# Kernel tuning notes

Measured on AMD Instinct MI355X. Metric: run time of the kernel, lower is better.

Reference implementation:

```python
import jax, jax.numpy as jnp
import numpy as np

B, L, D, H, F, NL = 112, 128, 768, 12, 3072, 3
E = D // H  # head dim = 64
BN_EPS = 1e-5


def _bn(x, gamma, beta):
    # torch BatchNorm1d applied on x.permute(0,2,1): per-channel (d_model) stats over batch+seq
    mean = jnp.mean(x, axis=(0, 1), keepdims=True)
    var = jnp.var(x, axis=(0, 1), keepdims=True)
    return (x - mean) * jax.lax.rsqrt(var + BN_EPS) * gamma + beta


def setup_inputs() -> dict:
    key = jax.random.key(0)
    ks = jax.random.split(key, 10)
    s = 0.02
    inp = {
        "x": jax.random.normal(ks[0], (B, L, D), jnp.float32),
        "attn_bias": jax.random.normal(ks[1], (B, L, L, H), jnp.float32) * 0.1,
        "Wq": jax.random.normal(ks[2], (NL, D, D), jnp.float32) * s,
        "bq": jnp.zeros((NL, D), jnp.float32),
        "Wk": jax.random.normal(ks[3], (NL, D, D), jnp.float32) * s,
        "bk": jnp.zeros((NL, D), jnp.float32),
        "Wv": jax.random.normal(ks[4], (NL, D, D), jnp.float32) * s,
        "bv": jnp.zeros((NL, D), jnp.float32),
        "Wo": jax.random.normal(ks[5], (NL, D, D), jnp.float32) * s,
        "bo": jnp.zeros((NL, D), jnp.float32),
        "W1": jax.random.normal(ks[6], (NL, F, D), jnp.float32) * s,  # conv1 k=1 == Linear
        "b1": jnp.zeros((NL, F), jnp.float32),
        "W2": jax.random.normal(ks[7], (NL, D, F), jnp.float32) * s,  # conv2 k=1 == Linear
        "b2": jnp.zeros((NL, D), jnp.float32),
        "g1": jnp.ones((NL, D), jnp.float32),
        "be1": jnp.zeros((NL, D), jnp.float32),
        "g2": jnp.ones((NL, D), jnp.float32),
        "be2": jnp.zeros((NL, D), jnp.float32),
        "gf": jnp.ones((D,), jnp.float32),
        "bef": jnp.zeros((D,), jnp.float32),
    }
    return inp


def reference(x, attn_bias, Wq, bq, Wk, bk, Wv, bv, Wo, bo,
              W1, b1, W2, b2, g1, be1, g2, be2, gf, bef):
    scale = 1.0 / float(np.sqrt(E))
    bias_bhls = jnp.transpose(attn_bias, (0, 3, 1, 2))  # [B,H,L,S]
    for l in range(NL):
        q = (x @ Wq[l].T + bq[l]).reshape(B, L, H, E)
        k = (x @ Wk[l].T + bk[l]).reshape(B, L, H, E)
        v = (x @ Wv[l].T + bv[l]).reshape(B, L, H, E)
        scores = jnp.einsum('blhe,bshe->bhls', q, k)  # O(L^2) score tensor
        A = jax.nn.softmax(scores * scale + bias_bhls, axis=-1)
        V = jnp.einsum('bhls,bshd->blhd', A, v).reshape(B, L, D)
        new_x = V @ Wo[l].T + bo[l]
        x = _bn(x + new_x, g1[l], be1[l])
        y = jax.nn.gelu(x @ W1[l].T + b1[l], approximate=False)
        y = y @ W2[l].T + b2[l]
        x = _bn(x + y, g2[l], be2[l])
    return _bn(x, gf, bef)  # Encoder final BatchNorm1d(d_model)
```

## Files before the change

### kernel.cpp

```cpp
#include <hip/hip_runtime.h>

#define NB 112
#define SEQ 128
#define DM 768
#define NH 12
#define HD 64
#define FF 3072
#define NLAYER 3
#define MTOK (NB*SEQ)
#define QKVN (3*DM)
#define HEADTOT (NB*NH)
#define QSZ ((size_t)HEADTOT*SEQ*HD)

typedef unsigned short u16;
typedef __attribute__((ext_vector_type(8))) short short8;
typedef __attribute__((ext_vector_type(4))) float f32x4;
typedef __attribute__((ext_vector_type(4))) unsigned short us4;

__device__ __forceinline__ u16 f2bf(float f){
  unsigned u = __builtin_bit_cast(unsigned, f);
  u += 0x7FFFu + ((u >> 16) & 1u);
  return (u16)(u >> 16);
}
__device__ __forceinline__ float bf2f(u16 b){
  unsigned u = ((unsigned)b) << 16;
  return __builtin_bit_cast(float, u);
}
__device__ __forceinline__ unsigned cvt_pk_bf16(float lo, float hi){
  unsigned r;
  asm("v_cvt_pk_bf16_f32 %0, %1, %2" : "=v"(r) : "v"(lo), "v"(hi));
  return r;
}
__device__ __forceinline__ float gelu_t(float x){
  const float t = -1.5957691216057308f * x * __builtin_fmaf(0.044715f, x*x, 1.0f);
  return __fdividef(x, 1.0f + __expf(t));
}

__device__ __forceinline__ void gl_lds16(const void* g, void* l){
  __builtin_amdgcn_global_load_lds((const __attribute__((address_space(1))) unsigned*)g,
                                   (__attribute__((address_space(3))) unsigned*)l, 16, 0, 0);
}

template<int EPI>
__global__ __launch_bounds__(512, 1)
void gemm_bt(const u16* __restrict__ A, const u16* __restrict__ W,
             const float* __restrict__ bias, u16* __restrict__ obf,
             float* __restrict__ of32, const u16* __restrict__ res,
             float* __restrict__ p1, float* __restrict__ p2,
             int M, int N, int K, int Nt, int TPB)
{
  __shared__ __align__(16) char smem[163840];
  const int tid = threadIdx.x;
  const int w = tid >> 6, lane = tid & 63;
  const int wm = w >> 2, wn = w & 3;
  const int fr = lane & 15, fg = lane >> 4;
  const int fko = fg * 8;
  const int grid = gridDim.x;
  const int q8 = grid >> 3, r8 = grid & 7;
  const int xcd = blockIdx.x & 7, pos = blockIdx.x >> 3;
  const int start = xcd < r8 ? xcd * (q8 + 1) : r8 * (q8 + 1) + (xcd - r8) * q8;
  const int swz = start + pos;
  const int nt = K >> 6;
  const int tot = TPB * nt;
  const int l3 = lane >> 3;
  const int k16s = ((lane & 7) ^ l3) * 8;
  int rowAK[2][2], rowBK[2][2];
  #pragma unroll
  for (int mh = 0; mh < 2; mh++)
    #pragma unroll
    for (int j = 0; j < 2; j++)
      rowAK[mh][j] = (mh*64 + j*128 + w*8 + l3) * K;
  #pragma unroll
  for (int h = 0; h < 2; h++)
    #pragma unroll
    for (int j = 0; j < 2; j++)
      rowBK[h][j] = (h*128 + (w + j*8)*8 + l3) * K;

  auto stA = [&](int s, int soff) {
    #pragma unroll
    for (int mh = 0; mh < 2; mh++) {
      char* d = smem + s*32768 + (mh*64 + w*8)*128;
      gl_lds16(A + (size_t)soff + rowAK[mh][0] + k16s, d);
      gl_lds16(A + (size_t)soff + rowAK[mh][1] + k16s, d + 16384);
    }
  };
  auto stB = [&](int s, int soff) {
    #pragma unroll
    for (int h = 0; h < 2; h++) {
      char* d = smem + 98304 + s*32768 + (h*128 + w*8)*128;
      gl_lds16(W + (size_t)soff + rowBK[h][0] + k16s, d);
      gl_lds16(W + (size_t)soff + rowBK[h][1] + k16s, d + 8192);
    }
  };
  const int axor = (fr & 7) << 4;
  auto rdA2 = [&](int s, int mh, int kh, int mf) -> short8 {
    const int row = wm*128 + mh*64 + mf*16 + fr;
    return *(const short8*)(smem + s*32768 + row*128 + (((kh*32 + fko)*2) ^ axor));
  };
  auto rdB2 = [&](int s, int kh, int nf) -> short8 {
    const int row = wn*64 + nf*16 + fr;
    return *(const short8*)(smem + 98304 + s*32768 + row*128 + (((kh*32 + fko)*2) ^ axor));
  };
  auto coord = [&](int r, int& bm, int& bn) {
    const int lin = swz * TPB + r;
    const int mI = lin / Nt;
    bm = mI * 256; bn = (lin - mI * Nt) * 256;
  };

  f32x4 acc[8][4] = {};

  auto epi = [&](int bm, int bn) {
    float bs[4] = {0,0,0,0}, bq[4] = {0,0,0,0};
    #pragma unroll
    for (int mi = 0; mi < 8; mi++) {
      #pragma unroll
      for (int ni = 0; ni < 4; ni++) {
        const int c = bn + wn*64 + ni*16 + fr;
        const int r0 = bm + wm*128 + (mi>>2)*64 + (mi&3)*16 + fg*4;
        const float bc = bias[c];
        float v[4];
        #pragma unroll
        for (int j = 0; j < 4; j++) v[j] = acc[mi][ni][j] + bc;
        if constexpr (EPI == 1) {
          #pragma unroll
          for (int j = 0; j < 4; j++) v[j] = gelu_t(v[j]);
          const unsigned p01 = cvt_pk_bf16(v[0], v[1]);
          const unsigned p23 = cvt_pk_bf16(v[2], v[3]);
          u16* d = obf + (size_t)r0 * N + c;
          d[0] = (u16)p01; d[N] = (u16)(p01 >> 16);
          d[2*N] = (u16)p23; d[3*N] = (u16)(p23 >> 16);
        } else if constexpr (EPI == 2) {
          #pragma unroll
          for (int j = 0; j < 4; j++) {
            const float y = v[j] + bf2f(res[(size_t)(r0+j) * N + c]);
            of32[(size_t)(r0+j) * N + c] = y;
            bs[ni] += y; bq[ni] += y * y;
          }
        } else {
          const int which = c / DM;
          const int cc = c - which * DM;
          const int hh = cc >> 6, e = cc & 63;
          const int bb = r0 >> 7, l = r0 & 127;
          const unsigned p01 = cvt_pk_bf16(v[0], v[1]);
          const unsigned p23 = cvt_pk_bf16(v[2], v[3]);
          u16* d = obf + (size_t)which * QSZ + ((size_t)(bb*NH + hh) * SEQ + l) * HD + e;
          d[0] = (u16)p01; d[HD] = (u16)(p01 >> 16);
          d[2*HD] = (u16)p23; d[3*HD] = (u16)(p23 >> 16);
        }
        acc[mi][ni] = (f32x4){0.f, 0.f, 0.f, 0.f};
      }
    }
    if constexpr (EPI == 2) {
      const int mIdx = bm >> 8;
      #pragma unroll
      for (int ni = 0; ni < 4; ni++) {
        float s = bs[ni], qq = bq[ni];
        s  += __shfl_xor(s, 16);  s  += __shfl_xor(s, 32);
        qq += __shfl_xor(qq, 16); qq += __shfl_xor(qq, 32);
        if (fg == 0) {
          const int c = bn + wn*64 + ni*16 + fr;
          p1[(mIdx*2 + wm) * N + c] = s;
          p2[(mIdx*2 + wm) * N + c] = qq;
        }
      }
    }
  };

  int r0t = 0, kt0 = 0, bm0, bn0; coord(0, bm0, bn0);
  int r1 = 0, kt1 = 1, bm1 = bm0, bn1 = bn0;
  int r2 = 0, kt2 = 2, bm2 = bm0;
  if (kt2 >= nt) { kt2 -= nt; r2 = 1; int d; if (r2 < TPB) coord(r2, bm2, d); }

  stA(0, bm0*K + kt0*64);
  stB(0, bn0*K + kt0*64);
  if (tot > 1) stA(1, bm1*K + kt1*64);
  asm volatile("s_waitcnt vmcnt(4)" ::: "memory");
  __builtin_amdgcn_s_barrier();

  short8 a0[4], a1[4], bk0[4], bk1[4];
  int bufA = 0;
  for (int it = 0; it < tot; ++it) {
    const int bufB = it & 1;
    int slA2 = bufA + 2; if (slA2 >= 3) slA2 -= 3;
    const int slB1 = bufB ^ 1;
    const bool st1 = (it + 1 < tot), st2 = (it + 2 < tot);
    const int sB1 = bn1*K + kt1*64;
    const int sA2 = bm2*K + kt2*64;
    #pragma unroll
    for (int i = 0; i < 4; i++) a0[i] = rdA2(bufA, 0, 0, i);
    #pragma unroll
    for (int i = 0; i < 4; i++) a1[i] = rdA2(bufA, 0, 1, i);
    #pragma unroll
    for (int i = 0; i < 4; i++) bk0[i] = rdB2(bufB, 0, i);
    #pragma unroll
    for (int i = 0; i < 4; i++) bk1[i] = rdB2(bufB, 1, i);
    if (st1) stB(slB1, sB1);
    if (st2) stA(slA2, sA2);
    asm volatile("s_waitcnt lgkmcnt(0)" ::: "memory");
    __builtin_amdgcn_sched_barrier(0);
    __builtin_amdgcn_s_setprio(1);
    #pragma unroll
    for (int mi = 0; mi < 4; mi++)
      #pragma unroll
      for (int ni = 0; ni < 4; ni++)
        acc[mi][ni] = __builtin_amdgcn_mfma_f32_16x16x32_bf16(a0[mi], bk0[ni], acc[mi][ni], 0, 0, 0);
    #pragma unroll
    for (int mi = 0; mi < 4; mi++)
      #pragma unroll
      for (int ni = 0; ni < 4; ni++)
        acc[mi][ni] = __builtin_amdgcn_mfma_f32_16x16x32_bf16(a1[mi], bk1[ni], acc[mi][ni], 0, 0, 0);
    __builtin_amdgcn_s_setprio(0);
    #pragma unroll
    for (int i = 0; i < 4; i++) a0[i] = rdA2(bufA, 1, 0, i);
    #pragma unroll
    for (int i = 0; i < 4; i++) a1[i] = rdA2(bufA, 1, 1, i);
    asm volatile("s_waitcnt lgkmcnt(0)" ::: "memory");
    __builtin_amdgcn_sched_barrier(0);
    __builtin_amdgcn_s_setprio(1);
    #pragma unroll
    for (int mi = 0; mi < 4; mi++)
      #pragma unroll
      for (int ni = 0; ni < 4; ni++)
        acc[4+mi][ni] = __builtin_amdgcn_mfma_f32_16x16x32_bf16(a0[mi], bk0[ni], acc[4+mi][ni], 0, 0, 0);
    #pragma unroll
    for (int mi = 0; mi < 4; mi++)
      #pragma unroll
      for (int ni = 0; ni < 4; ni++)
        acc[4+mi][ni] = __builtin_amdgcn_mfma_f32_16x16x32_bf16(a1[mi], bk1[ni], acc[4+mi][ni], 0, 0, 0);
    __builtin_amdgcn_s_setprio(0);
    if (st2)      { asm volatile("s_waitcnt vmcnt(4)" ::: "memory"); }
    else if (st1) { asm volatile("s_waitcnt vmcnt(0)" ::: "memory"); }
    __builtin_amdgcn_s_barrier();
    if (kt0 == nt - 1) {
      epi(bm0, bn0);
      kt0 = 0; r0t++;
      if (r0t < TPB) coord(r0t, bm0, bn0);
    } else kt0++;
    kt1++; if (kt1 == nt) { kt1 = 0; r1++; if (r1 < TPB) coord(r1, bm1, bn1); }
    kt2++; if (kt2 == nt) { kt2 = 0; r2++; if (r2 < TPB) { int d; coord(r2, bm2, d); } }
    bufA++; if (bufA == 3) bufA = 0;
  }
}

__global__ __launch_bounds__(256)
void attn_kernel(const u16* __restrict__ qkvb, const u16* __restrict__ biasT,
                 u16* __restrict__ ab)
{
  const int h = blockIdx.x, b = blockIdx.y;
  const int tid = threadIdx.x, w = tid >> 6, lane = tid & 63;
  const int bh = b * NH + h;
  const u16* qp = qkvb + (size_t)bh * SEQ * HD;
  const u16* kp = qkvb + QSZ + (size_t)bh * SEQ * HD;
  const u16* vp = qkvb + 2 * QSZ + (size_t)bh * SEQ * HD;
  __shared__ __align__(16) u16 vT[HD * 136];
  __shared__ __align__(16) u16 P[SEQ * 136];
  {
    const int s = tid & 127, half = tid >> 7;
    #pragma unroll
    for (int rr = 0; rr < 4; rr++) {
      const int e0 = half * 32 + rr * 8;
      short8 v8 = *(const short8*)&vp[s * HD + e0];
      #pragma unroll
      for (int j = 0; j < 8; j++) vT[(e0 + j) * 136 + s] = (u16)v8[j];
    }
  }
  const int fr = lane & 15, fg = lane >> 4;
  f32x4 sacc[2][8] = {};
  #pragma unroll
  for (int ks = 0; ks < 2; ks++) {
    const int k0 = ks * 32 + fg * 8;
    short8 qf[2], kf[8];
    #pragma unroll
    for (int mi = 0; mi < 2; mi++) qf[mi] = *(const short8*)&qp[(w*32 + mi*16 + fr) * HD + k0];
    #pragma unroll
    for (int ni = 0; ni < 8; ni++) kf[ni] = *(const short8*)&kp[(ni*16 + fr) * HD + k0];
    #pragma unroll
    for (int mi = 0; mi < 2; mi++)
      #pragma unroll
      for (int ni = 0; ni < 8; ni++)
        sacc[mi][ni] = __builtin_amdgcn_mfma_f32_16x16x32_bf16(qf[mi], kf[ni], sacc[mi][ni], 0, 0, 0);
  }
  const u16* bt = biasT + (size_t)bh * SEQ * SEQ;
  #pragma unroll
  for (int mi = 0; mi < 2; mi++) {
    #pragma unroll
    for (int j = 0; j < 4; j++) {
      const int l = w*32 + mi*16 + fg*4 + j;
      float vals[8];
      float mx = -1e30f;
      #pragma unroll
      for (int ni = 0; ni < 8; ni++) {
        vals[ni] = sacc[mi][ni][j] * 0.125f + bf2f(bt[l * SEQ + ni*16 + fr]);
        mx = fmaxf(mx, vals[ni]);
      }
      #pragma unroll
      for (int d = 1; d < 16; d <<= 1) mx = fmaxf(mx, __shfl_xor(mx, d));
      float sum = 0.f;
      #pragma unroll
      for (int ni = 0; ni < 8; ni++) { vals[ni] = __expf(vals[ni] - mx); sum += vals[ni]; }
      #pragma unroll
      for (int d = 1; d < 16; d <<= 1) sum += __shfl_xor(sum, d);
      const float inv = 1.0f / sum;
      #pragma unroll
      for (int ni = 0; ni < 8; ni++) P[l * 136 + ni*16 + fr] = f2bf(vals[ni] * inv);
    }
  }
  __syncthreads();
  f32x4 oacc[2][4] = {};
  #pragma unroll
  for (int ss = 0; ss < 4; ss++) {
    const int s0 = ss * 32 + fg * 8;
    short8 pf[2], vf[4];
    #pragma unroll
    for (int mi = 0; mi < 2; mi++) pf[mi] = *(const short8*)&P[(w*32 + mi*16 + fr) * 136 + s0];
    #pragma unroll
    for (int ei = 0; ei < 4; ei++) vf[ei] = *(const short8*)&vT[(ei*16 + fr) * 136 + s0];
    #pragma unroll
    for (int mi = 0; mi < 2; mi++)
      #pragma unroll
      for (int ei = 0; ei < 4; ei++)
        oacc[mi][ei] = __builtin_amdgcn_mfma_f32_16x16x32_bf16(pf[mi], vf[ei], oacc[mi][ei], 0, 0, 0);
  }
  #pragma unroll
  for (int mi = 0; mi < 2; mi++)
    #pragma unroll
    for (int ei = 0; ei < 4; ei++)
      #pragma unroll
      for (int j = 0; j < 4; j++) {
        const int r = b * SEQ + w*32 + mi*16 + fg*4 + j;
        const int c = h * HD + ei*16 + fr;
        ab[(size_t)r * DM + c] = f2bf(oacc[mi][ei][j]);
      }
}

template<bool FINAL>
__global__ __launch_bounds__(256)
void bn_final(const float* __restrict__ p1, const float* __restrict__ p2,
              const float* __restrict__ ga, const float* __restrict__ be,
              const float* __restrict__ gb, const float* __restrict__ beb,
              float* __restrict__ sc, float* __restrict__ sh)
{
  const int c = blockIdx.x * 256 + threadIdx.x;
  float s = 0, q = 0;
  for (int i = 0; i < 112; i++) { s += p1[i * DM + c]; q += p2[i * DM + c]; }
  const float mean = s * (1.0f / MTOK);
  const float var = q * (1.0f / MTOK) - mean * mean;
  const float rstd = rsqrtf(var + 1e-5f);
  if constexpr (!FINAL) {
    const float g = ga[c] * rstd;
    sc[c] = g;
    sh[c] = be[c] - mean * g;
  } else {
    const float sc2 = ga[c] * rstd;
    const float sh2 = be[c] - mean * sc2;
    const float varf = sc2 * sc2 * var;
    const float meanf = sc2 * mean + sh2;
    const float scf = gb[c] * rsqrtf(varf + 1e-5f);
    const float shf = beb[c] - meanf * scf;
    sc[c] = scf * sc2;
    sh[c] = scf * sh2 + shf;
  }
}

template<int MODE>
__global__ __launch_bounds__(256)
void bn_apply(const float* __restrict__ xi, const float* __restrict__ sc,
              const float* __restrict__ sh, float* __restrict__ xo, u16* __restrict__ xb)
{
  const int i = blockIdx.x * 256 + threadIdx.x;
  const int c0 = (i % (DM / 8)) * 2;
  float4 v0 = ((const float4*)xi)[i*2];
  float4 v1 = ((const float4*)xi)[i*2 + 1];
  const float4 s0 = ((const float4*)sc)[c0];
  const float4 s1 = ((const float4*)sc)[c0 + 1];
  const float4 h0 = ((const float4*)sh)[c0];
  const float4 h1 = ((const float4*)sh)[c0 + 1];
  float y0x = __builtin_fmaf(v0.x, s0.x, h0.x), y0y = __builtin_fmaf(v0.y, s0.y, h0.y);
  float y0z = __builtin_fmaf(v0.z, s0.z, h0.z), y0w = __builtin_fmaf(v0.w, s0.w, h0.w);
  float y1x = __builtin_fmaf(v1.x, s1.x, h1.x), y1y = __builtin_fmaf(v1.y, s1.y, h1.y);
  float y1z = __builtin_fmaf(v1.z, s1.z, h1.z), y1w = __builtin_fmaf(v1.w, s1.w, h1.w);
  if constexpr (MODE == 1) {
    ((float4*)xo)[i*2]     = (float4){y0x, y0y, y0z, y0w};
    ((float4*)xo)[i*2 + 1] = (float4){y1x, y1y, y1z, y1w};
  } else {
    short8 r;
    unsigned pA = cvt_pk_bf16(y0x, y0y), pB = cvt_pk_bf16(y0z, y0w);
    unsigned pC = cvt_pk_bf16(y1x, y1y), pD = cvt_pk_bf16(y1z, y1w);
    r[0] = (short)(u16)pA; r[1] = (short)(u16)(pA >> 16);
    r[2] = (short)(u16)pB; r[3] = (short)(u16)(pB >> 16);
    r[4] = (short)(u16)pC; r[5] = (short)(u16)(pC >> 16);
    r[6] = (short)(u16)pD; r[7] = (short)(u16)(pD >> 16);
    *(short8*)&xb[(size_t)i * 8] = r;
  }
}

__global__ __launch_bounds__(256)
void conv_bf16(const float* __restrict__ s, u16* __restrict__ d, int n8)
{
  const int i = blockIdx.x * 256 + threadIdx.x;
  if (i >= n8) return;
  float4 v0 = ((const float4*)s)[i*2];
  float4 v1 = ((const float4*)s)[i*2 + 1];
  short8 r;
  unsigned pA = cvt_pk_bf16(v0.x, v0.y), pB = cvt_pk_bf16(v0.z, v0.w);
  unsigned pC = cvt_pk_bf16(v1.x, v1.y), pD = cvt_pk_bf16(v1.z, v1.w);
  r[0] = (short)(u16)pA; r[1] = (short)(u16)(pA >> 16);
  r[2] = (short)(u16)pB; r[3] = (short)(u16)(pB >> 16);
  r[4] = (short)(u16)pC; r[5] = (short)(u16)(pC >> 16);
  r[6] = (short)(u16)pD; r[7] = (short)(u16)(pD >> 16);
  *(short8*)&d[(size_t)i * 8] = r;
}

__global__ __launch_bounds__(256)
void conv_qkvw(const float* __restrict__ wq, const float* __restrict__ wk,
               const float* __restrict__ wv, u16* __restrict__ d)
{
  const int i = blockIdx.x * 256 + threadIdx.x;
  const int per = QKVN * DM / 8;
  const int l = i / per;
  const int rem = i - l * per;
  const int r = rem / (DM / 8);
  const int cv = rem - r * (DM / 8);
  const float* srcrow;
  if (r < DM)          srcrow = wq + ((size_t)l * DM + r) * DM;
  else if (r < 2 * DM) srcrow = wk + ((size_t)l * DM + (r - DM)) * DM;
  else                 srcrow = wv + ((size_t)l * DM + (r - 2 * DM)) * DM;
  float4 v0 = ((const float4*)srcrow)[cv*2];
  float4 v1 = ((const float4*)srcrow)[cv*2 + 1];
  short8 o;
  unsigned pA = cvt_pk_bf16(v0.x, v0.y), pB = cvt_pk_bf16(v0.z, v0.w);
  unsigned pC = cvt_pk_bf16(v1.x, v1.y), pD = cvt_pk_bf16(v1.z, v1.w);
  o[0] = (short)(u16)pA; o[1] = (short)(u16)(pA >> 16);
  o[2] = (short)(u16)pB; o[3] = (short)(u16)(pB >> 16);
  o[4] = (short)(u16)pC; o[5] = (short)(u16)(pC >> 16);
  o[6] = (short)(u16)pD; o[7] = (short)(u16)(pD >> 16);
  *(short8*)&d[(size_t)i * 8] = o;
}

__global__ __launch_bounds__(256)
void conv_bias_qkv(const float* __restrict__ bq, const float* __restrict__ bk,
                   const float* __restrict__ bv, float* __restrict__ d)
{
  const int i = blockIdx.x * 256 + threadIdx.x;
  const int l = i / QKVN;
  const int r = i - l * QKVN;
  float v;
  if (r < DM)          v = bq[l * DM + r];
  else if (r < 2 * DM) v = bk[l * DM + r - DM];
  else                 v = bv[l * DM + r - 2 * DM];
  d[i] = v;
}

__global__ __launch_bounds__(256)
void bias_tr(const float* __restrict__ src, u16* __restrict__ dst)
{
  const int l = blockIdx.x, b = blockIdx.y;
  __shared__ float row[SEQ * NH];
  const float* s = src + ((size_t)b * SEQ + l) * SEQ * NH;
  for (int i = threadIdx.x; i < SEQ * NH; i += 256) row[i] = s[i];
  __syncthreads();
  for (int i = threadIdx.x; i < SEQ * NH; i += 256) {
    const int h = i >> 7, ss = i & 127;
    dst[((size_t)(b * NH + h) * SEQ + l) * SEQ + ss] = f2bf(row[ss * NH + h]);
  }
}

extern "C" void kernel_launch(void* const* d_in, const int* in_sizes, int n_in,
                              void* d_out, int out_size, void* d_ws, size_t ws_size,
                              hipStream_t stream)
{
  const float* x    = (const float*)d_in[0];
  const float* abia = (const float*)d_in[1];
  const float* Wq   = (const float*)d_in[2];
  const float* bq   = (const float*)d_in[3];
  const float* Wk   = (const float*)d_in[4];
  const float* bk   = (const float*)d_in[5];
  const float* Wv   = (const float*)d_in[6];
  const float* bv   = (const float*)d_in[7];
  const float* Wo   = (const float*)d_in[8];
  const float* bo   = (const float*)d_in[9];
  const float* W1   = (const float*)d_in[10];
  const float* b1   = (const float*)d_in[11];
  const float* W2   = (const float*)d_in[12];
  const float* b2   = (const float*)d_in[13];
  const float* g1   = (const float*)d_in[14];
  const float* be1  = (const float*)d_in[15];
  const float* g2   = (const float*)d_in[16];
  const float* be2  = (const float*)d_in[17];
  const float* gf   = (const float*)d_in[18];
  const float* bef  = (const float*)d_in[19];
  float* out = (float*)d_out;

  char* ws = (char*)d_ws;
  size_t off = 0;
  auto alloc = [&](size_t n) -> char* {
    char* p = ws + off;
    off = (off + n + 255) & ~(size_t)255;
    return p;
  };
  u16*  wqkv  = (u16*)alloc((size_t)3 * QKVN * DM * 2);
  u16*  wo    = (u16*)alloc((size_t)3 * DM * DM * 2);
  u16*  w1    = (u16*)alloc((size_t)3 * FF * DM * 2);
  u16*  w2    = (u16*)alloc((size_t)3 * DM * FF * 2);
  float* bqkv = (float*)alloc((size_t)3 * QKVN * 4);
  u16*  xb    = (u16*)alloc((size_t)MTOK * DM * 2);
  u16*  ab    = (u16*)alloc((size_t)MTOK * DM * 2);
  u16*  big   = (u16*)alloc((size_t)MTOK * FF * 2);
  u16*  biasT = (u16*)alloc((size_t)HEADTOT * SEQ * SEQ * 2);
  float* p1   = (float*)alloc((size_t)112 * DM * 4);
  float* p2   = (float*)alloc((size_t)112 * DM * 4);
  float* sc   = (float*)alloc(DM * 4);
  float* sh   = (float*)alloc(DM * 4);
  if (off > ws_size) return;

  conv_qkvw<<<2592, 256, 0, stream>>>(Wq, Wk, Wv, wqkv);
  conv_bf16<<<864, 256, 0, stream>>>(Wo, wo, 3 * DM * DM / 8);
  conv_bf16<<<3456, 256, 0, stream>>>(W1, w1, 3 * FF * DM / 8);
  conv_bf16<<<3456, 256, 0, stream>>>(W2, w2, 3 * DM * FF / 8);
  conv_bias_qkv<<<27, 256, 0, stream>>>(bq, bk, bv, bqkv);
  bias_tr<<<dim3(SEQ, NB), 256, 0, stream>>>(abia, biasT);
  conv_bf16<<<MTOK * DM / 8 / 256, 256, 0, stream>>>(x, xb, MTOK * DM / 8);

  auto gemm = [&](int epi, const u16* Ap, const u16* Wp, const float* bp,
                  u16* ob, float* o32, const u16* rs, int M, int N, int K) {
    const int Nt = N / 256;
    const int tiles = (M / 256) * Nt;
    const int tpb = (tiles + 255) / 256;
    const int grid = tiles / tpb;
    if (epi == 1)
      gemm_bt<1><<<grid, 512, 0, stream>>>(Ap, Wp, bp, ob, o32, rs, p1, p2, M, N, K, Nt, tpb);
    else if (epi == 2)
      gemm_bt<2><<<grid, 512, 0, stream>>>(Ap, Wp, bp, ob, o32, rs, p1, p2, M, N, K, Nt, tpb);
    else
      gemm_bt<3><<<grid, 512, 0, stream>>>(Ap, Wp, bp, ob, o32, rs, p1, p2, M, N, K, Nt, tpb);
  };

  for (int l = 0; l < NLAYER; l++) {
    gemm(3, xb, wqkv + (size_t)l * QKVN * DM, bqkv + l * QKVN, big, nullptr, nullptr,
         MTOK, QKVN, DM);
    attn_kernel<<<dim3(NH, NB), 256, 0, stream>>>(big, biasT, ab);
    gemm(2, ab, wo + (size_t)l * DM * DM, bo + l * DM, nullptr, out, xb,
         MTOK, DM, DM);
    bn_final<false><<<3, 256, 0, stream>>>(p1, p2, g1 + l * DM, be1 + l * DM,
                                           nullptr, nullptr, sc, sh);
    bn_apply<0><<<MTOK * DM / 8 / 256, 256, 0, stream>>>(out, sc, sh, nullptr, xb);
    gemm(1, xb, w1 + (size_t)l * FF * DM, b1 + l * FF, big, nullptr, nullptr,
         MTOK, FF, DM);
    gemm(2, big, w2 + (size_t)l * DM * FF, b2 + l * DM, nullptr, out, xb,
         MTOK, DM, FF);
    if (l < NLAYER - 1) {
      bn_final<false><<<3, 256, 0, stream>>>(p1, p2, g2 + l * DM, be2 + l * DM,
                                             nullptr, nullptr, sc, sh);
      bn_apply<0><<<MTOK * DM / 8 / 256, 256, 0, stream>>>(out, sc, sh, nullptr, xb);
    } else {
      bn_final<true><<<3, 256, 0, stream>>>(p1, p2, g2 + l * DM, be2 + l * DM,
                                            gf, bef, sc, sh);
      bn_apply<1><<<MTOK * DM / 8 / 256, 256, 0, stream>>>(out, sc, sh, out, nullptr);
    }
  }
}
```

Baseline: 1.132 ms.

## Switch GEMM to 128x128 tiles with 256-thread blocks, two per CU

Rewrites the persistent bf16 GEMM to use 128x128 output tiles computed by 4 waves of 256 threads, with half the LDS, so two blocks can share a CU. It launches a fixed grid of 512 blocks and spreads tiles evenly across them, XCD-aware, instead of grouping whole 256x256 tiles per block. The aim is better load balance and occupancy, and less tail imbalance on the 256-tile grids. The cost is lower data reuse per tile, meaning more global and LDS traffic per flop. BN partial sums now cover 224 row blocks, and the workspace and reduction are resized to match.

```diff
diff --git a/kernel.cpp b/kernel.cpp
--- a/kernel.cpp
+++ b/kernel.cpp
@@ -42,82 +42,67 @@
 }
 
 template<int EPI>
-__global__ __launch_bounds__(512, 1)
+__global__ __launch_bounds__(256, 2)
 void gemm_bt(const u16* __restrict__ A, const u16* __restrict__ W,
              const float* __restrict__ bias, u16* __restrict__ obf,
              float* __restrict__ of32, const u16* __restrict__ res,
              float* __restrict__ p1, float* __restrict__ p2,
-             int M, int N, int K, int Nt, int TPB)
-{
-  __shared__ __align__(16) char smem[163840];
+             int M, int N, int K, int Nt, int tiles)
+{
+  __shared__ __align__(16) char smem[81920];
   const int tid = threadIdx.x;
   const int w = tid >> 6, lane = tid & 63;
-  const int wm = w >> 2, wn = w & 3;
+  const int wm = w >> 1, wn = w & 1;
   const int fr = lane & 15, fg = lane >> 4;
-  const int fko = fg * 8;
-  const int grid = gridDim.x;
-  const int q8 = grid >> 3, r8 = grid & 7;
   const int xcd = blockIdx.x & 7, pos = blockIdx.x >> 3;
-  const int start = xcd < r8 ? xcd * (q8 + 1) : r8 * (q8 + 1) + (xcd - r8) * q8;
-  const int swz = start + pos;
+  const int swz = xcd * 64 + pos;
+  const int q = tiles >> 9, e = tiles & 511;
+  const int startT = swz * q + (swz < e ? swz : e);
+  const int myT = q + (swz < e ? 1 : 0);
   const int nt = K >> 6;
-  const int tot = TPB * nt;
-  const int l3 = lane >> 3;
-  const int k16s = ((lane & 7) ^ l3) * 8;
-  int rowAK[2][2], rowBK[2][2];
+  const int tot = myT * nt;
+  const int rowt = tid >> 3;
+  const int k16s = ((tid & 7) ^ (rowt & 7)) * 8;
+  int rowK[4];
   #pragma unroll
-  for (int mh = 0; mh < 2; mh++)
-    #pragma unroll
-    for (int j = 0; j < 2; j++)
-      rowAK[mh][j] = (mh*64 + j*128 + w*8 + l3) * K;
-  #pragma unroll
-  for (int h = 0; h < 2; h++)
-    #pragma unroll
-    for (int j = 0; j < 2; j++)
-      rowBK[h][j] = (h*128 + (w + j*8)*8 + l3) * K;
+  for (int j = 0; j < 4; j++) rowK[j] = (j*32 + rowt) * K;
 
   auto stA = [&](int s, int soff) {
     #pragma unroll
-    for (int mh = 0; mh < 2; mh++) {
-      char* d = smem + s*32768 + (mh*64 + w*8)*128;
-      gl_lds16(A + (size_t)soff + rowAK[mh][0] + k16s, d);
-      gl_lds16(A + (size_t)soff + rowAK[mh][1] + k16s, d + 16384);
-    }
+    for (int j = 0; j < 4; j++)
+      gl_lds16(A + (size_t)soff + rowK[j] + k16s, smem + s*16384 + j*4096 + tid*16);
   };
   auto stB = [&](int s, int soff) {
     #pragma unroll
-    for (int h = 0; h < 2; h++) {
-      char* d = smem + 98304 + s*32768 + (h*128 + w*8)*128;
-      gl_lds16(W + (size_t)soff + rowBK[h][0] + k16s, d);
-      gl_lds16(W + (size_t)soff + rowBK[h][1] + k16s, d + 8192);
-    }
+    for (int j = 0; j < 4; j++)
+      gl_lds16(W + (size_t)soff + rowK[j] + k16s, smem + 49152 + s*16384 + j*4096 + tid*16);
   };
   const int axor = (fr & 7) << 4;
-  auto rdA2 = [&](int s, int mh, int kh, int mf) -> short8 {
-    const int row = wm*128 + mh*64 + mf*16 + fr;
-    return *(const short8*)(smem + s*32768 + row*128 + (((kh*32 + fko)*2) ^ axor));
-  };
-  auto rdB2 = [&](int s, int kh, int nf) -> short8 {
+  auto rdA = [&](int s, int kh, int mf) -> short8 {
+    const int row = wm*64 + mf*16 + fr;
+    return *(const short8*)(smem + s*16384 + row*128 + (((kh*32 + fg*8)*2) ^ axor));
+  };
+  auto rdB = [&](int s, int kh, int nf) -> short8 {
     const int row = wn*64 + nf*16 + fr;
-    return *(const short8*)(smem + 98304 + s*32768 + row*128 + (((kh*32 + fko)*2) ^ axor));
+    return *(const short8*)(smem + 49152 + s*16384 + row*128 + (((kh*32 + fg*8)*2) ^ axor));
   };
   auto coord = [&](int r, int& bm, int& bn) {
-    const int lin = swz * TPB + r;
+    const int lin = startT + r;
     const int mI = lin / Nt;
-    bm = mI * 256; bn = (lin - mI * Nt) * 256;
-  };
-
-  f32x4 acc[8][4] = {};
+    bm = mI * 128; bn = (lin - mI * Nt) * 128;
+  };
+
+  f32x4 acc[4][4] = {};
 
   auto epi = [&](int bm, int bn) {
     float bs[4] = {0,0,0,0}, bq[4] = {0,0,0,0};
     #pragma unroll
-    for (int mi = 0; mi < 8; mi++) {
-      #pragma unroll
-      for (int ni = 0; ni < 4; ni++) {
-        const int c = bn + wn*64 + ni*16 + fr;
-        const int r0 = bm + wm*128 + (mi>>2)*64 + (mi&3)*16 + fg*4;
-        const float bc = bias[c];
+    for (int ni = 0; ni < 4; ni++) {
+      const int c = bn + wn*64 + ni*16 + fr;
+      const float bc = bias[c];
+      #pragma unroll
+      for (int mi = 0; mi < 4; mi++) {
+        const int r0 = bm + wm*64 + mi*16 + fg*4;
         float v[4];
         #pragma unroll
         for (int j = 0; j < 4; j++) v[j] = acc[mi][ni][j] + bc;
@@ -139,11 +124,11 @@
         } else {
           const int which = c / DM;
           const int cc = c - which * DM;
-          const int hh = cc >> 6, e = cc & 63;
+          const int hh = cc >> 6, ee = cc & 63;
           const int bb = r0 >> 7, l = r0 & 127;
           const unsigned p01 = cvt_pk_bf16(v[0], v[1]);
           const unsigned p23 = cvt_pk_bf16(v[2], v[3]);
-          u16* d = obf + (size_t)which * QSZ + ((size_t)(bb*NH + hh) * SEQ + l) * HD + e;
+          u16* d = obf + (size_t)which * QSZ + ((size_t)(bb*NH + hh) * SEQ + l) * HD + ee;
           d[0] = (u16)p01; d[HD] = (u16)(p01 >> 16);
           d[2*HD] = (u16)p23; d[3*HD] = (u16)(p23 >> 16);
         }
@@ -151,7 +136,7 @@
       }
     }
     if constexpr (EPI == 2) {
-      const int mIdx = bm >> 8;
+      const int mIdx = bm >> 7;
       #pragma unroll
       for (int ni = 0; ni < 4; ni++) {
         float s = bs[ni], qq = bq[ni];
@@ -169,7 +154,8 @@
   int r0t = 0, kt0 = 0, bm0, bn0; coord(0, bm0, bn0);
   int r1 = 0, kt1 = 1, bm1 = bm0, bn1 = bn0;
   int r2 = 0, kt2 = 2, bm2 = bm0;
-  if (kt2 >= nt) { kt2 -= nt; r2 = 1; int d; if (r2 < TPB) coord(r2, bm2, d); }
+  if (kt1 >= nt) { kt1 -= nt; r1 = 1; if (r1 < myT) coord(r1, bm1, bn1); }
+  if (kt2 >= nt) { kt2 -= nt; r2 = 1; int d; if (r2 < myT) coord(r2, bm2, d); }
 
   stA(0, bm0*K + kt0*64);
   stB(0, bn0*K + kt0*64);
@@ -177,7 +163,7 @@
   asm volatile("s_waitcnt vmcnt(4)" ::: "memory");
   __builtin_amdgcn_s_barrier();
 
-  short8 a0[4], a1[4], bk0[4], bk1[4];
+  short8 a0[4], a1[4], b0[4], b1[4];
   int bufA = 0;
   for (int it = 0; it < tot; ++it) {
     const int bufB = it & 1;
@@ -187,13 +173,13 @@
     const int sB1 = bn1*K + kt1*64;
     const int sA2 = bm2*K + kt2*64;
     #pragma unroll
-    for (int i = 0; i < 4; i++) a0[i] = rdA2(bufA, 0, 0, i);
-    #pragma unroll
-    for (int i = 0; i < 4; i++) a1[i] = rdA2(bufA, 0, 1, i);
-    #pragma unroll
-    for (int i = 0; i < 4; i++) bk0[i] = rdB2(bufB, 0, i);
-    #pragma unroll
-    for (int i = 0; i < 4; i++) bk1[i] = rdB2(bufB, 1, i);
+    for (int i = 0; i < 4; i++) a0[i] = rdA(bufA, 0, i);
+    #pragma unroll
+    for (int i = 0; i < 4; i++) a1[i] = rdA(bufA, 1, i);
+    #pragma unroll
+    for (int i = 0; i < 4; i++) b0[i] = rdB(bufB, 0, i);
+    #pragma unroll
+    for (int i = 0; i < 4; i++) b1[i] = rdB(bufB, 1, i);
     if (st1) stB(slB1, sB1);
     if (st2) stA(slA2, sA2);
     asm volatile("s_waitcnt lgkmcnt(0)" ::: "memory");
@@ -203,30 +189,12 @@
     for (int mi = 0; mi < 4; mi++)
       #pragma unroll
       for (int ni = 0; ni < 4; ni++)
-        acc[mi][ni] = __builtin_amdgcn_mfma_f32_16x16x32_bf16(a0[mi], bk0[ni], acc[mi][ni], 0, 0, 0);
+        acc[mi][ni] = __builtin_amdgcn_mfma_f32_16x16x32_bf16(a0[mi], b0[ni], acc[mi][ni], 0, 0, 0);
     #pragma unroll
     for (int mi = 0; mi < 4; mi++)
       #pragma unroll
       for (int ni = 0; ni < 4; ni++)
-        acc[mi][ni] = __builtin_amdgcn_mfma_f32_16x16x32_bf16(a1[mi], bk1[ni], acc[mi][ni], 0, 0, 0);
-    __builtin_amdgcn_s_setprio(0);
-    #pragma unroll
-    for (int i = 0; i < 4; i++) a0[i] = rdA2(bufA, 1, 0, i);
-    #pragma unroll
-    for (int i = 0; i < 4; i++) a1[i] = rdA2(bufA, 1, 1, i);
-    asm volatile("s_waitcnt lgkmcnt(0)" ::: "memory");
-    __builtin_amdgcn_sched_barrier(0);
-    __builtin_amdgcn_s_setprio(1);
-    #pragma unroll
-    for (int mi = 0; mi < 4; mi++)
-      #pragma unroll
-      for (int ni = 0; ni < 4; ni++)
-        acc[4+mi][ni] = __builtin_amdgcn_mfma_f32_16x16x32_bf16(a0[mi], bk0[ni], acc[4+mi][ni], 0, 0, 0);
-    #pragma unroll
-    for (int mi = 0; mi < 4; mi++)
-      #pragma unroll
-      for (int ni = 0; ni < 4; ni++)
-        acc[4+mi][ni] = __builtin_amdgcn_mfma_f32_16x16x32_bf16(a1[mi], bk1[ni], acc[4+mi][ni], 0, 0, 0);
+        acc[mi][ni] = __builtin_amdgcn_mfma_f32_16x16x32_bf16(a1[mi], b1[ni], acc[mi][ni], 0, 0, 0);
     __builtin_amdgcn_s_setprio(0);
     if (st2)      { asm volatile("s_waitcnt vmcnt(4)" ::: "memory"); }
     else if (st1) { asm volatile("s_waitcnt vmcnt(0)" ::: "memory"); }
@@ -234,10 +202,10 @@
     if (kt0 == nt - 1) {
       epi(bm0, bn0);
       kt0 = 0; r0t++;
-      if (r0t < TPB) coord(r0t, bm0, bn0);
+      if (r0t < myT) coord(r0t, bm0, bn0);
     } else kt0++;
-    kt1++; if (kt1 == nt) { kt1 = 0; r1++; if (r1 < TPB) coord(r1, bm1, bn1); }
-    kt2++; if (kt2 == nt) { kt2 = 0; r2++; if (r2 < TPB) { int d; coord(r2, bm2, d); } }
+    kt1++; if (kt1 == nt) { kt1 = 0; r1++; if (r1 < myT) coord(r1, bm1, bn1); }
+    kt2++; if (kt2 == nt) { kt2 = 0; r2++; if (r2 < myT) { int d; coord(r2, bm2, d); } }
     bufA++; if (bufA == 3) bufA = 0;
   }
 }
@@ -342,7 +310,7 @@
 {
   const int c = blockIdx.x * 256 + threadIdx.x;
   float s = 0, q = 0;
-  for (int i = 0; i < 112; i++) { s += p1[i * DM + c]; q += p2[i * DM + c]; }
+  for (int i = 0; i < 224; i++) { s += p1[i * DM + c]; q += p2[i * DM + c]; }
   const float mean = s * (1.0f / MTOK);
   const float var = q * (1.0f / MTOK) - mean * mean;
   const float rstd = rsqrtf(var + 1e-5f);
@@ -507,8 +475,8 @@
   u16*  ab    = (u16*)alloc((size_t)MTOK * DM * 2);
   u16*  big   = (u16*)alloc((size_t)MTOK * FF * 2);
   u16*  biasT = (u16*)alloc((size_t)HEADTOT * SEQ * SEQ * 2);
-  float* p1   = (float*)alloc((size_t)112 * DM * 4);
-  float* p2   = (float*)alloc((size_t)112 * DM * 4);
+  float* p1   = (float*)alloc((size_t)224 * DM * 4);
+  float* p2   = (float*)alloc((size_t)224 * DM * 4);
   float* sc   = (float*)alloc(DM * 4);
   float* sh   = (float*)alloc(DM * 4);
   if (off > ws_size) return;
@@ -523,16 +491,14 @@
 
   auto gemm = [&](int epi, const u16* Ap, const u16* Wp, const float* bp,
                   u16* ob, float* o32, const u16* rs, int M, int N, int K) {
-    const int Nt = N / 256;
-    const int tiles = (M / 256) * Nt;
-    const int tpb = (tiles + 255) / 256;
-    const int grid = tiles / tpb;
+    const int Nt = N / 128;
+    const int tiles = (M / 128) * Nt;
     if (epi == 1)
-      gemm_bt<1><<<grid, 512, 0, stream>>>(Ap, Wp, bp, ob, o32, rs, p1, p2, M, N, K, Nt, tpb);
+      gemm_bt<1><<<512, 256, 0, stream>>>(Ap, Wp, bp, ob, o32, rs, p1, p2, M, N, K, Nt, tiles);
     else if (epi == 2)
-      gemm_bt<2><<<grid, 512, 0, stream>>>(Ap, Wp, bp, ob, o32, rs, p1, p2, M, N, K, Nt, tpb);
+      gemm_bt<2><<<512, 256, 0, stream>>>(Ap, Wp, bp, ob, o32, rs, p1, p2, M, N, K, Nt, tiles);
     else
-      gemm_bt<3><<<grid, 512, 0, stream>>>(Ap, Wp, bp, ob, o32, rs, p1, p2, M, N, K, Nt, tpb);
+      gemm_bt<3><<<512, 256, 0, stream>>>(Ap, Wp, bp, ob, o32, rs, p1, p2, M, N, K, Nt, tiles);
   };
 
   for (int l = 0; l < NLAYER; l++) {
```

New measurement: 1.230 ms. 1.09x slower.
